# Performance work log

Measured on AMD Instinct MI355X. Metric: run time of the kernel, lower is better.

## Reference

```python
import jax, jax.numpy as jnp
import numpy as np

K = 3          # deform conv kernel size
PAD = 1        # (K-1)//2
DG = 4         # deformable groups
C_IN = 256     # sum(in_channel_list)
C_OUT = 256


def setup_inputs() -> dict:
    key = jax.random.key(0)
    k0, k1, k2, k3, k4, k5 = jax.random.split(key, 6)
    B, H, W = 2, 64, 256
    x0 = jax.random.normal(k0, (B, 64, H, W), dtype=jnp.float32)
    x1 = jax.random.normal(k1, (B, 64, H, W), dtype=jnp.float32)
    x2 = jax.random.normal(k2, (B, 128, H, W), dtype=jnp.float32)
    # conv_offset: 1x1 conv, weight zero-inited in the module; we use small
    # random weights so offsets are spatially varying (nontrivial sampling).
    w_off = jax.random.normal(k3, (DG * K * K * 2, C_IN), dtype=jnp.float32) * 0.01
    b_off = jax.random.normal(k4, (DG * K * K * 2,), dtype=jnp.float32) * 0.5
    # deform conv weight [O, C, K*K] (flat kernel, row-major i*K+j), no bias (mmcv DeformConv)
    w_def = jax.random.normal(k5, (C_OUT, C_IN, K * K), dtype=jnp.float32) / np.sqrt(C_IN * K * K)
    return {"x0": x0, "x1": x1, "x2": x2, "w_off": w_off, "b_off": b_off, "w_def": w_def}


def _deform_gather(xg, py, px):
    # xg: [B, DG, Cg, H, W] grouped input; py/px: [B, DG, K2, H, W] abs sample coords
    B, dg, Cg, H, W = xg.shape
    K2 = py.shape[2]
    y0f = jnp.floor(py)
    x0f = jnp.floor(px)
    wy = py - y0f  # fractional parts
    wx = px - x0f
    y0 = y0f.astype(jnp.int32)
    x0 = x0f.astype(jnp.int32)
    xf = xg.reshape(B, dg, Cg, H * W)

    def corner(yi, xi, w):
        valid = ((yi >= 0) & (yi <= H - 1) & (xi >= 0) & (xi <= W - 1)).astype(xg.dtype)
        idx = jnp.clip(yi, 0, H - 1) * W + jnp.clip(xi, 0, W - 1)   # [B,dg,K2,H,W]
        idxf = idx.reshape(B, dg, 1, K2 * H * W)
        g = jnp.take_along_axis(xf, jnp.broadcast_to(idxf, (B, dg, Cg, K2 * H * W)), axis=-1)
        g = g.reshape(B, dg, Cg, K2, H, W)
        return g * (w * valid)[:, :, None]  # broadcast over Cg

    return (corner(y0, x0, (1.0 - wy) * (1.0 - wx))
            + corner(y0, x0 + 1, (1.0 - wy) * wx)
            + corner(y0 + 1, x0, wy * (1.0 - wx))
            + corner(y0 + 1, x0 + 1, wy * wx))  # [B,dg,Cg,K2,H,W]


def reference(x0, x1, x2, w_off, b_off, w_def):
    x = jnp.concatenate([x0, x1, x2], axis=1)  # [B, C, H, W]
    B, C, H, W = x.shape
    # 1x1 offset conv
    off = jnp.einsum('bchw,oc->bohw', x, w_off) + b_off[None, :, None, None]
    off = off.reshape(B, DG, K * K, 2, H, W)
    dy = off[:, :, :, 0]  # [B,DG,K2,H,W]
    dx = off[:, :, :, 1]
    ky, kx = jnp.meshgrid(jnp.arange(K), jnp.arange(K), indexing='ij')
    ky = ky.reshape(-1).astype(jnp.float32)
    kx = kx.reshape(-1).astype(jnp.float32)
    hh = jnp.arange(H, dtype=jnp.float32)
    ww = jnp.arange(W, dtype=jnp.float32)
    py = hh[None, None, None, :, None] - PAD + ky[None, None, :, None, None] + dy
    px = ww[None, None, None, None, :] - PAD + kx[None, None, :, None, None] + dx
    xg = x.reshape(B, DG, C // DG, H, W)
    samp = _deform_gather(xg, py, px).reshape(B, C, K * K, H, W)
    out = jnp.einsum('bckhw,ock->bohw', samp, w_def)
    return jax.nn.relu(out)
```

## Files before the change

kernel.cpp:

```cpp
#include <hip/hip_runtime.h>


constexpr int H_ = 64, W_ = 256;
constexpr int HWsz = H_ * W_;
constexpr int OC_ = 256;
constexpr int WMAIN_ELEMS = 72 * 16 * 64 * 8;
constexpr int WOFFB_ELEMS = 8 * 5 * 64 * 8;
constexpr size_t XT_ELEMS = (size_t)8 * HWsz * 64;

using f32x4 = __attribute__((ext_vector_type(4))) float;
using s16x8 = __attribute__((ext_vector_type(8))) short;
using u16x8 = __attribute__((ext_vector_type(8))) unsigned short;

__device__ __forceinline__ unsigned short f2bf(float f) {
    unsigned u = __float_as_uint(f);
    return (unsigned short)((u + 0x7fffu + ((u >> 16) & 1u)) >> 16);
}
__device__ __forceinline__ float bf2f(unsigned short u) {
    return __uint_as_float((unsigned)u << 16);
}
__device__ __forceinline__ unsigned cvt_pk_bf16(float lo, float hi) {
    unsigned r;
    asm("v_cvt_pk_bf16_f32 %0, %1, %2" : "=v"(r) : "v"(lo), "v"(hi));
    return r;
}
__device__ __forceinline__ void gload_lds16(const void* g, void* l) {
    __builtin_amdgcn_global_load_lds(
        (const __attribute__((address_space(1))) void*)g,
        (__attribute__((address_space(3))) void*)l, 16, 0, 0);
}


__global__ __launch_bounds__(256) void wprep_kernel(const float* __restrict__ w_def,
                                                    const float* __restrict__ w_off,
                                                    unsigned short* __restrict__ w2) {
    int i = blockIdx.x * 256 + threadIdx.x;
    if (i < WMAIN_ELEMS) {
        int j = i & 7, lane = (i >> 3) & 63, t = (i >> 9) & 15, gkh = i >> 13;
        int half = gkh & 1, gk = gkh >> 1;
        int k = gk % 9, g = gk / 9;
        int oc = t * 16 + (lane & 15);
        int cin = g * 64 + half * 32 + (lane >> 4) * 8 + j;
        w2[i] = f2bf(w_def[(size_t)oc * 2304 + (size_t)cin * 9 + k]);
    } else if (i < WMAIN_ELEMS + WOFFB_ELEMS) {
        int i2 = i - WMAIN_ELEMS;
        int j = i2 & 7, lane = (i2 >> 3) & 63, idx = i2 >> 9;
        int t = idx % 5, c8 = idx / 5;
        int o = t * 16 + (lane & 15);
        int ch = c8 * 32 + (lane >> 4) * 8 + j;
        float v = (o < 72) ? w_off[o * 256 + ch] : 0.f;
        w2[i] = f2bf(v);
    }
}

__global__ __launch_bounds__(256) void xprep_kernel(const float* __restrict__ x0,
                                                    const float* __restrict__ x1,
                                                    const float* __restrict__ x2,
                                                    unsigned short* __restrict__ xt) {
    __shared__ unsigned short tl[256][66];
    const int bg = blockIdx.x >> 6;
    const int y  = blockIdx.x & 63;
    const int b  = bg >> 2, g = bg & 3;
    const int tid = threadIdx.x;
    const float* src = (g == 0) ? x0 + (size_t)b * 64 * HWsz
                     : (g == 1) ? x1 + (size_t)b * 64 * HWsz
                     : x2 + (size_t)b * 128 * HWsz + (size_t)(g - 2) * 64 * HWsz;
    src += y * W_;
    for (int c = 0; c < 64; ++c)
        tl[tid][c] = f2bf(src[(size_t)c * HWsz + tid]);
    __syncthreads();
    unsigned short* dst = xt + ((size_t)bg * HWsz + y * W_) * 64;
    #pragma unroll
    for (int s = 0; s < 8; ++s) {
        int si = s * 256 + tid;
        int px = si >> 3, q = si & 7;
        u16x8 v;
        #pragma unroll
        for (int j = 0; j < 8; ++j) v[j] = tl[px][q * 8 + j];
        *(u16x8*)(dst + (size_t)px * 64 + q * 8) = v;
    }
}


struct GPre {
    float w00, w01, w10, w11;
    u16x8 c00, c01, c10, c11;
};

__global__ __launch_bounds__(512, 4) void deform64_kernel(
    const unsigned short* __restrict__ xt, const float* __restrict__ b_off,
    const unsigned short* __restrict__ w2, float* __restrict__ out)
{
    __shared__ float off_lds[72 * 64];
    __shared__ __align__(16) unsigned short Bbuf[16384];
    __shared__ __align__(16) unsigned short sbuf16[8192];

    const int tid  = threadIdx.x;
    const int lane = tid & 63;
    const int wv   = tid >> 6;
    const int bid  = ((blockIdx.x & 7) << 6) | (blockIdx.x >> 3);
    const int xt4  = bid & 3;
    const int h    = (bid >> 2) & 63;
    const int b    = bid >> 8;
    const int xbase = xt4 * 64;
    const int nh   = wv & 1;
    const int pg   = wv >> 1;
    const int p16  = lane & 15;
    const int cq   = lane >> 4;
    const int bp   = wv * 8 + (lane >> 3);
    const int chg  = lane & 7;
    const int halfw = chg >> 2;
    const int cqw   = chg & 3;
    const int slotw = ((cqw << 4) | (bp & 15)) ^ cqw ^ (halfw << 2);
    const int sbw   = halfw * 2048 + (bp >> 4) * 512 + slotw * 8;
    const int roff0 = pg * 512 + (lane ^ cq) * 8;
    const int roff1 = 2048 + pg * 512 + (lane ^ cq ^ 4) * 8;

    const unsigned short* xtb = xt + (size_t)b * 4 * HWsz * 64;

    if (wv < 4) {
        f32x4 oa[5];
        #pragma unroll
        for (int t = 0; t < 5; ++t) {
            int o = t * 16 + p16;
            float bv = (o < 72) ? b_off[o] : 0.f;
            oa[t][0] = bv; oa[t][1] = bv; oa[t][2] = bv; oa[t][3] = bv;
        }
        const int pixg = h * W_ + xbase + wv * 16;
        #pragma unroll
        for (int c8 = 0; c8 < 8; ++c8) {
            const unsigned short* ap = xtb + (size_t)(c8 >> 1) * HWsz * 64
                                     + (size_t)(pixg + p16) * 64 + (c8 & 1) * 32 + cq * 8;
            s16x8 a = *(const s16x8*)ap;
            const unsigned short* wb = w2 + WMAIN_ELEMS + (size_t)(c8 * 5) * 512;
            #pragma unroll
            for (int t = 0; t < 5; ++t) {
                s16x8 bf = *(const s16x8*)(wb + t * 512 + lane * 8);
                oa[t] = __builtin_amdgcn_mfma_f32_16x16x32_bf16(a, bf, oa[t], 0, 0, 0);
            }
        }
        #pragma unroll
        for (int t = 0; t < 5; ++t) {
            int o = t * 16 + p16;
            if (o < 72) {
                #pragma unroll
                for (int r = 0; r < 4; ++r)
                    off_lds[o * 64 + wv * 16 + cq * 4 + r] = oa[t][r];
            }
        }
    }
    __syncthreads();

    auto stageB = [&](int gk) {
        const char* src = (const char*)w2 + (size_t)gk * 32768 + (size_t)tid * 16;
        char* dst = (char*)&Bbuf[0] + wv * 1024;
        #pragma unroll
        for (int q = 0; q < 4; ++q)
            gload_lds16(src + q * 8192, dst + q * 8192);
    };
    auto gpre = [&](int gk) -> GPre {
        const int k = gk % 9, g = gk / 9;
        const int ky = k / 3, kx = k % 3;
        float dy = off_lds[(2 * gk) * 64 + bp];
        float dx = off_lds[(2 * gk + 1) * 64 + bp];
        float fy = (float)(h - 1 + ky) + dy;
        float fx = (float)(xbase + bp - 1 + kx) + dx;
        float y0f = floorf(fy), x0f = floorf(fx);
        float wy = fy - y0f, wx = fx - x0f;
        int iy0 = (int)y0f, ix0 = (int)x0f;
        int iy1 = iy0 + 1, ix1 = ix0 + 1;
        float vy0 = (iy0 >= 0 && iy0 < H_) ? 1.f : 0.f;
        float vy1 = (iy1 >= 0 && iy1 < H_) ? 1.f : 0.f;
        float vx0 = (ix0 >= 0 && ix0 < W_) ? 1.f : 0.f;
        float vx1 = (ix1 >= 0 && ix1 < W_) ? 1.f : 0.f;
        GPre G;
        G.w00 = (1.f - wy) * (1.f - wx) * vy0 * vx0;
        G.w01 = (1.f - wy) * wx * vy0 * vx1;
        G.w10 = wy * (1.f - wx) * vy1 * vx0;
        G.w11 = wy * wx * vy1 * vx1;
        int cy0 = min(max(iy0, 0), H_ - 1), cy1 = min(max(iy1, 0), H_ - 1);
        int cx0 = min(max(ix0, 0), W_ - 1), cx1 = min(max(ix1, 0), W_ - 1);
        const unsigned short* src = xtb + (size_t)g * HWsz * 64 + chg * 8;
        G.c00 = *(const u16x8*)(src + (cy0 * W_ + cx0) * 64);
        G.c01 = *(const u16x8*)(src + (cy0 * W_ + cx1) * 64);
        G.c10 = *(const u16x8*)(src + (cy1 * W_ + cx0) * 64);
        G.c11 = *(const u16x8*)(src + (cy1 * W_ + cx1) * 64);
        return G;
    };
    auto gpost = [&](const GPre& G, int buf) {
        unsigned d[4];
        #pragma unroll
        for (int q = 0; q < 4; ++q) {
            float v0 = fmaf(G.w00, bf2f(G.c00[2*q]), fmaf(G.w01, bf2f(G.c01[2*q]),
                       fmaf(G.w10, bf2f(G.c10[2*q]), G.w11 * bf2f(G.c11[2*q]))));
            float v1 = fmaf(G.w00, bf2f(G.c00[2*q+1]), fmaf(G.w01, bf2f(G.c01[2*q+1]),
                       fmaf(G.w10, bf2f(G.c10[2*q+1]), G.w11 * bf2f(G.c11[2*q+1]))));
            d[q] = cvt_pk_bf16(v0, v1);
        }
        uint4 v4; v4.x = d[0]; v4.y = d[1]; v4.z = d[2]; v4.w = d[3];
        *(uint4*)&sbuf16[buf * 4096 + sbw] = v4;
    };

    f32x4 acc[8];
    #pragma unroll
    for (int t = 0; t < 8; ++t) { acc[t][0]=0; acc[t][1]=0; acc[t][2]=0; acc[t][3]=0; }

    stageB(0);
    {
        GPre G0 = gpre(0);
        gpost(G0, 0);
    }
    GPre G = gpre(1);

    for (int i = 0; i < 36; ++i) {
        __syncthreads();
        const int cur = i & 1;
        const unsigned short* sb = sbuf16 + cur * 4096;
        {
            s16x8 a = *(const s16x8*)(sb + roff0);
            const unsigned short* bb = Bbuf + nh * 4096 + lane * 8;
            #pragma unroll
            for (int t = 0; t < 8; ++t) {
                s16x8 bf = *(const s16x8*)(bb + t * 512);
                acc[t] = __builtin_amdgcn_mfma_f32_16x16x32_bf16(a, bf, acc[t], 0, 0, 0);
            }
        }
        {
            s16x8 a = *(const s16x8*)(sb + roff1);
            const unsigned short* bb = Bbuf + 8192 + nh * 4096 + lane * 8;
            #pragma unroll
            for (int t = 0; t < 8; ++t) {
                s16x8 bf = *(const s16x8*)(bb + t * 512);
                acc[t] = __builtin_amdgcn_mfma_f32_16x16x32_bf16(a, bf, acc[t], 0, 0, 0);
            }
        }
        if (i < 35) gpost(G, cur ^ 1);
        __syncthreads();
        if (i < 35) stageB(i + 1);
        if (i < 34) G = gpre(i + 2);
    }

    const size_t obase = (size_t)b * OC_ * HWsz + (size_t)h * W_
                       + xbase + pg * 16 + cq * 4;
    #pragma unroll
    for (int t = 0; t < 8; ++t) {
        int oc = nh * 128 + t * 16 + p16;
        float4 r;
        r.x = fmaxf(acc[t][0], 0.f);
        r.y = fmaxf(acc[t][1], 0.f);
        r.z = fmaxf(acc[t][2], 0.f);
        r.w = fmaxf(acc[t][3], 0.f);
        *(float4*)(out + obase + (size_t)oc * HWsz) = r;
    }
}


struct Geom {
    float w00, w01, w10, w11;
    int o00, o01, o10, o11;
    const float* base;
};

__device__ __forceinline__ Geom make_geom(
    int gkh, const float* offp, int h, int wbase, int p, int cq,
    const float* xA, const float* xB, const float* xC)
{
    const int half = gkh & 1, gk = gkh >> 1;
    const int k = gk % 9, g = gk / 9;
    const int ky = k / 3, kx = k % 3;
    float dy = offp[(2 * gk) * 16 + p];
    float dx = offp[(2 * gk + 1) * 16 + p];
    float fy = (float)(h - 1 + ky) + dy;
    float fx = (float)(wbase + p - 1 + kx) + dx;
    float y0f = floorf(fy), x0f = floorf(fx);
    float wy = fy - y0f, wx = fx - x0f;
    int iy0 = (int)y0f, ix0 = (int)x0f;
    int iy1 = iy0 + 1, ix1 = ix0 + 1;
    float vy0 = (iy0 >= 0 && iy0 < H_) ? 1.f : 0.f;
    float vy1 = (iy1 >= 0 && iy1 < H_) ? 1.f : 0.f;
    float vx0 = (ix0 >= 0 && ix0 < W_) ? 1.f : 0.f;
    float vx1 = (ix1 >= 0 && ix1 < W_) ? 1.f : 0.f;
    Geom gm;
    gm.w00 = (1.f - wy) * (1.f - wx) * vy0 * vx0;
    gm.w01 = (1.f - wy) * wx * vy0 * vx1;
    gm.w10 = wy * (1.f - wx) * vy1 * vx0;
    gm.w11 = wy * wx * vy1 * vx1;
    int cy0 = min(max(iy0, 0), H_ - 1), cy1 = min(max(iy1, 0), H_ - 1);
    int cx0 = min(max(ix0, 0), W_ - 1), cx1 = min(max(ix1, 0), W_ - 1);
    int choff = (half * 32 + cq * 8) * HWsz;
    gm.o00 = choff + cy0 * W_ + cx0;
    gm.o01 = choff + cy0 * W_ + cx1;
    gm.o10 = choff + cy1 * W_ + cx0;
    gm.o11 = choff + cy1 * W_ + cx1;
    gm.base = (g == 0) ? xA : (g == 1) ? xB : (g == 2) ? xC : xC + (size_t)64 * HWsz;
    return gm;
}

#define GATHER(J, Cv) do { \
    Cv.x = gm.base[gm.o00 + (J) * HWsz]; \
    Cv.y = gm.base[gm.o01 + (J) * HWsz]; \
    Cv.z = gm.base[gm.o10 + (J) * HWsz]; \
    Cv.w = gm.base[gm.o11 + (J) * HWsz]; \
} while (0)

#define COMB(Cv, IDX) \
    a[IDX] = (short)f2bf(fmaf(w00c, Cv.x, fmaf(w01c, Cv.y, fmaf(w10c, Cv.z, w11c * Cv.w))))

template<bool USE_WS>
__global__ __launch_bounds__(128, 3) void deform_kernel(
    const float* __restrict__ x0, const float* __restrict__ x1,
    const float* __restrict__ x2,
    const float* __restrict__ w_off, const float* __restrict__ b_off,
    const float* __restrict__ w_def, const unsigned short* __restrict__ w2,
    float* __restrict__ out)
{
    __shared__ float off_lds[2][72 * 16];

    const int tid  = threadIdx.x;
    const int lane = tid & 63;
    const int wv   = tid >> 6;
    const int bid  = ((blockIdx.x & 7) << 8) | (blockIdx.x >> 3);
    const int nh   = wv;
    const int ws_  = bid & 15;
    const int h    = (bid >> 4) & 63;
    const int b    = bid >> 10;
    const int p    = lane & 15;
    const int cq   = lane >> 4;
    const int wbase = ws_ * 16;
    const int pix  = h * W_ + wbase;

    const float* xA = x0 + (size_t)b * 64  * HWsz;
    const float* xB = x1 + (size_t)b * 64  * HWsz;
    const float* xC = x2 + (size_t)b * 128 * HWsz;

    f32x4 oa[5];
    #pragma unroll
    for (int t = 0; t < 5; ++t) {
        int o = t * 16 + p;
        float bv = (o < 72) ? b_off[o] : 0.f;
        oa[t][0] = bv; oa[t][1] = bv; oa[t][2] = bv; oa[t][3] = bv;
    }
    #pragma unroll
    for (int c8 = 0; c8 < 8; ++c8) {
        const float* src = (c8 < 2) ? xA + (size_t)c8 * 32 * HWsz
                         : (c8 < 4) ? xB + (size_t)(c8 - 2) * 32 * HWsz
                                    : xC + (size_t)(c8 - 4) * 32 * HWsz;
        s16x8 a;
        #pragma unroll
        for (int j = 0; j < 8; ++j)
            a[j] = (short)f2bf(src[(cq * 8 + j) * HWsz + pix + p]);
        #pragma unroll
        for (int t = 0; t < 5; ++t) {
            int o = t * 16 + p;
            s16x8 bf;
            if (USE_WS) {
                bf = *(const s16x8*)(w2 + WMAIN_ELEMS + (size_t)(c8 * 5 + t) * 512 + lane * 8);
            } else {
                #pragma unroll
                for (int j = 0; j < 8; ++j)
                    bf[j] = (o < 72) ? (short)f2bf(w_off[o * 256 + c8 * 32 + cq * 8 + j])
                                     : (short)0;
            }
            oa[t] = __builtin_amdgcn_mfma_f32_16x16x32_bf16(a, bf, oa[t], 0, 0, 0);
        }
    }
    #pragma unroll
    for (int t = 0; t < 5; ++t) {
        int o = t * 16 + p;
        if (o < 72) {
            #pragma unroll
            for (int r = 0; r < 4; ++r)
                off_lds[wv][o * 16 + cq * 4 + r] = oa[t][r];
        }
    }

    f32x4 acc0={0,0,0,0},acc1={0,0,0,0},acc2={0,0,0,0},acc3={0,0,0,0};
    f32x4 acc4={0,0,0,0},acc5={0,0,0,0},acc6={0,0,0,0},acc7={0,0,0,0};
    const float* offp = &off_lds[wv][0];

    for (int gkh = 0; gkh < 72; ++gkh) {
        Geom gm = make_geom(gkh, offp, h, wbase, p, cq, xA, xB, xC);
        float4 c0, c1, c2, c3, c4, c5, c6, c7;
        GATHER(0, c0); GATHER(1, c1); GATHER(2, c2); GATHER(3, c3);
        GATHER(4, c4); GATHER(5, c5); GATHER(6, c6); GATHER(7, c7);
        float w00c = gm.w00, w01c = gm.w01, w10c = gm.w10, w11c = gm.w11;
        s16x8 a;
        COMB(c0, 0); COMB(c1, 1); COMB(c2, 2); COMB(c3, 3);
        COMB(c4, 4); COMB(c5, 5); COMB(c6, 6); COMB(c7, 7);
        const int half = gkh & 1, gk = gkh >> 1;
        const int k = gk % 9, g = gk / 9;
        const int cbase = g * 64 + half * 32 + cq * 8;
        f32x4* accp[8] = {&acc0,&acc1,&acc2,&acc3,&acc4,&acc5,&acc6,&acc7};
        #pragma unroll
        for (int t = 0; t < 8; ++t) {
            int oc = nh * 128 + t * 16 + p;
            s16x8 bf;
            if (USE_WS) {
                bf = *(const s16x8*)(w2 + gkh * 8192 + nh * 4096 + t * 512 + lane * 8);
            } else {
                #pragma unroll
                for (int j = 0; j < 8; ++j)
                    bf[j] = (short)f2bf(w_def[(size_t)oc * 2304 + (size_t)(cbase + j) * 9 + k]);
            }
            *accp[t] = __builtin_amdgcn_mfma_f32_16x16x32_bf16(a, bf, *accp[t], 0, 0, 0);
        }
    }

    const size_t obase = (size_t)b * OC_ * HWsz + (size_t)h * W_ + wbase + cq * 4;
    f32x4 accs[8] = {acc0, acc1, acc2, acc3, acc4, acc5, acc6, acc7};
    #pragma unroll
    for (int t = 0; t < 8; ++t) {
        int oc = nh * 128 + t * 16 + p;
        float4 r;
        r.x = fmaxf(accs[t][0], 0.f);
        r.y = fmaxf(accs[t][1], 0.f);
        r.z = fmaxf(accs[t][2], 0.f);
        r.w = fmaxf(accs[t][3], 0.f);
        *(float4*)(out + obase + (size_t)oc * HWsz) = r;
    }
}

extern "C" void kernel_launch(void* const* d_in, const int* in_sizes, int n_in,
                              void* d_out, int out_size, void* d_ws, size_t ws_size,
                              hipStream_t stream) {
    const float* x0    = (const float*)d_in[0];
    const float* x1    = (const float*)d_in[1];
    const float* x2    = (const float*)d_in[2];
    const float* w_off = (const float*)d_in[3];
    const float* b_off = (const float*)d_in[4];
    const float* w_def = (const float*)d_in[5];
    float* out = (float*)d_out;

    const size_t w2_bytes   = (size_t)(WMAIN_ELEMS + WOFFB_ELEMS) * 2;
    const size_t full_bytes = (XT_ELEMS + WMAIN_ELEMS + WOFFB_ELEMS) * 2;

    if (ws_size >= full_bytes) {
        unsigned short* xt = (unsigned short*)d_ws;
        unsigned short* w2 = xt + XT_ELEMS;
        hipLaunchKernelGGL(xprep_kernel, dim3(512), dim3(256), 0, stream, x0, x1, x2, xt);
        hipLaunchKernelGGL(wprep_kernel, dim3((WMAIN_ELEMS + WOFFB_ELEMS) / 256), dim3(256),
                           0, stream, w_def, w_off, w2);
        hipLaunchKernelGGL(deform64_kernel, dim3(512), dim3(512), 0, stream,
                           xt, b_off, w2, out);
    } else if (ws_size >= w2_bytes) {
        unsigned short* w2 = (unsigned short*)d_ws;
        hipLaunchKernelGGL(wprep_kernel, dim3((WMAIN_ELEMS + WOFFB_ELEMS) / 256), dim3(256),
                           0, stream, w_def, w_off, w2);
        hipLaunchKernelGGL((deform_kernel<true>), dim3(2048), dim3(128), 0, stream,
                           x0, x1, x2, w_off, b_off, w_def, w2, out);
    } else {
        hipLaunchKernelGGL((deform_kernel<false>), dim3(2048), dim3(128), 0, stream,
                           x0, x1, x2, w_off, b_off, w_def, (const unsigned short*)nullptr, out);
    }
}
```

Before: 91.09 us.

## Precompute packed bilinear geometry in LDS and use packed FP32 FMA for interpolation

```diff
diff --git a/kernel.cpp b/kernel.cpp
--- a/kernel.cpp
+++ b/kernel.cpp
@@ -9,6 +9,7 @@
 constexpr size_t XT_ELEMS = (size_t)8 * HWsz * 64;
 
 using f32x4 = __attribute__((ext_vector_type(4))) float;
+using f32x2 = __attribute__((ext_vector_type(2))) float;
 using s16x8 = __attribute__((ext_vector_type(8))) short;
 using u16x8 = __attribute__((ext_vector_type(8))) unsigned short;
 
@@ -22,6 +23,22 @@
 __device__ __forceinline__ unsigned cvt_pk_bf16(float lo, float hi) {
     unsigned r;
     asm("v_cvt_pk_bf16_f32 %0, %1, %2" : "=v"(r) : "v"(lo), "v"(hi));
+    return r;
+}
+__device__ __forceinline__ f32x2 pk_fma(f32x2 a, f32x2 b, f32x2 c) {
+    f32x2 d;
+    asm("v_pk_fma_f32 %0, %1, %2, %3" : "=v"(d) : "v"(a), "v"(b), "v"(c));
+    return d;
+}
+__device__ __forceinline__ f32x2 pk_mul(f32x2 a, f32x2 b) {
+    f32x2 d;
+    asm("v_pk_mul_f32 %0, %1, %2" : "=v"(d) : "v"(a), "v"(b));
+    return d;
+}
+__device__ __forceinline__ f32x2 unpk_bf(unsigned u) {
+    f32x2 r;
+    r[0] = __uint_as_float(u << 16);
+    r[1] = __uint_as_float(u & 0xffff0000u);
     return r;
 }
 __device__ __forceinline__ void gload_lds16(const void* g, void* l) {
@@ -91,7 +108,7 @@
     const unsigned short* __restrict__ xt, const float* __restrict__ b_off,
     const unsigned short* __restrict__ w2, float* __restrict__ out)
 {
-    __shared__ float off_lds[72 * 64];
+    __shared__ __align__(8) unsigned geomLds[2 * 2304];
     __shared__ __align__(16) unsigned short Bbuf[16384];
     __shared__ __align__(16) unsigned short sbuf16[8192];
 
@@ -118,6 +135,7 @@
 
     const unsigned short* xtb = xt + (size_t)b * 4 * HWsz * 64;
 
+    float* tmpoff = (float*)&Bbuf[0];
     if (wv < 4) {
         f32x4 oa[5];
         #pragma unroll
@@ -145,26 +163,20 @@
             if (o < 72) {
                 #pragma unroll
                 for (int r = 0; r < 4; ++r)
-                    off_lds[o * 64 + wv * 16 + cq * 4 + r] = oa[t][r];
+                    tmpoff[o * 64 + wv * 16 + cq * 4 + r] = oa[t][r];
             }
         }
     }
     __syncthreads();
 
-    auto stageB = [&](int gk) {
-        const char* src = (const char*)w2 + (size_t)gk * 32768 + (size_t)tid * 16;
-        char* dst = (char*)&Bbuf[0] + wv * 1024;
-        #pragma unroll
-        for (int q = 0; q < 4; ++q)
-            gload_lds16(src + q * 8192, dst + q * 8192);
-    };
-    auto gpre = [&](int gk) -> GPre {
-        const int k = gk % 9, g = gk / 9;
+    for (int idx = tid; idx < 36 * 64; idx += 512) {
+        const int gk = idx >> 6, p = idx & 63;
+        const int k = gk % 9;
         const int ky = k / 3, kx = k % 3;
-        float dy = off_lds[(2 * gk) * 64 + bp];
-        float dx = off_lds[(2 * gk + 1) * 64 + bp];
+        float dy = tmpoff[(2 * gk) * 64 + p];
+        float dx = tmpoff[(2 * gk + 1) * 64 + p];
         float fy = (float)(h - 1 + ky) + dy;
-        float fx = (float)(xbase + bp - 1 + kx) + dx;
+        float fx = (float)(xbase + p - 1 + kx) + dx;
         float y0f = floorf(fy), x0f = floorf(fx);
         float wy = fy - y0f, wx = fx - x0f;
         int iy0 = (int)y0f, ix0 = (int)x0f;
@@ -173,31 +185,73 @@
         float vy1 = (iy1 >= 0 && iy1 < H_) ? 1.f : 0.f;
         float vx0 = (ix0 >= 0 && ix0 < W_) ? 1.f : 0.f;
         float vx1 = (ix1 >= 0 && ix1 < W_) ? 1.f : 0.f;
-        GPre G;
-        G.w00 = (1.f - wy) * (1.f - wx) * vy0 * vx0;
-        G.w01 = (1.f - wy) * wx * vy0 * vx1;
-        G.w10 = wy * (1.f - wx) * vy1 * vx0;
-        G.w11 = wy * wx * vy1 * vx1;
+        float w00 = (1.f - wy) * (1.f - wx) * vy0 * vx0;
+        float w01 = (1.f - wy) * wx * vy0 * vx1;
+        float w10 = wy * (1.f - wx) * vy1 * vx0;
+        float w11 = wy * wx * vy1 * vx1;
         int cy0 = min(max(iy0, 0), H_ - 1), cy1 = min(max(iy1, 0), H_ - 1);
         int cx0 = min(max(ix0, 0), W_ - 1), cx1 = min(max(ix1, 0), W_ - 1);
+        unsigned q00 = (unsigned)(w00 * 2047.f + 0.5f);
+        unsigned q01 = (unsigned)(w01 * 2047.f + 0.5f);
+        unsigned q10 = (unsigned)(w10 * 2047.f + 0.5f);
+        unsigned q11 = (unsigned)(w11 * 2047.f + 0.5f);
+        unsigned lo = q00 | (q01 << 11) | ((unsigned)cy0 << 22)
+                    | ((unsigned)(cy1 - cy0) << 28);
+        unsigned hi = q10 | (q11 << 11) | ((unsigned)cx0 << 22)
+                    | ((unsigned)(cx1 - cx0) << 30);
+        geomLds[idx * 2]     = lo;
+        geomLds[idx * 2 + 1] = hi;
+    }
+    __syncthreads();
+
+    auto stageB = [&](int gk) {
+        const char* src = (const char*)w2 + (size_t)gk * 32768 + (size_t)tid * 16;
+        char* dst = (char*)&Bbuf[0] + wv * 1024;
+        #pragma unroll
+        for (int q = 0; q < 4; ++q)
+            gload_lds16(src + q * 8192, dst + q * 8192);
+    };
+    auto gpre = [&](int gk) -> GPre {
+        const int g = gk / 9;
+        const unsigned lo = geomLds[(gk * 64 + bp) * 2];
+        const unsigned hi = geomLds[(gk * 64 + bp) * 2 + 1];
+        GPre G;
+        constexpr float S = 1.f / 2047.f;
+        G.w00 = (float)(lo & 2047u) * S;
+        G.w01 = (float)((lo >> 11) & 2047u) * S;
+        G.w10 = (float)(hi & 2047u) * S;
+        G.w11 = (float)((hi >> 11) & 2047u) * S;
+        const int cy0 = (lo >> 22) & 63;
+        const int cx0 = (hi >> 22) & 255;
+        const int dy1 = ((lo >> 28) & 1) << 14;
+        const int dx1 = ((hi >> 30) & 1) << 6;
+        const int o00 = (cy0 << 14) + (cx0 << 6);
         const unsigned short* src = xtb + (size_t)g * HWsz * 64 + chg * 8;
-        G.c00 = *(const u16x8*)(src + (cy0 * W_ + cx0) * 64);
-        G.c01 = *(const u16x8*)(src + (cy0 * W_ + cx1) * 64);
-        G.c10 = *(const u16x8*)(src + (cy1 * W_ + cx0) * 64);
-        G.c11 = *(const u16x8*)(src + (cy1 * W_ + cx1) * 64);
+        G.c00 = *(const u16x8*)(src + o00);
+        G.c01 = *(const u16x8*)(src + o00 + dx1);
+        G.c10 = *(const u16x8*)(src + o00 + dy1);
+        G.c11 = *(const u16x8*)(src + o00 + dy1 + dx1);
         return G;
     };
     auto gpost = [&](const GPre& G, int buf) {
-        unsigned d[4];
-        #pragma unroll
-        for (int q = 0; q < 4; ++q) {
-            float v0 = fmaf(G.w00, bf2f(G.c00[2*q]), fmaf(G.w01, bf2f(G.c01[2*q]),
-                       fmaf(G.w10, bf2f(G.c10[2*q]), G.w11 * bf2f(G.c11[2*q]))));
-            float v1 = fmaf(G.w00, bf2f(G.c00[2*q+1]), fmaf(G.w01, bf2f(G.c01[2*q+1]),
-                       fmaf(G.w10, bf2f(G.c10[2*q+1]), G.w11 * bf2f(G.c11[2*q+1]))));
-            d[q] = cvt_pk_bf16(v0, v1);
-        }
-        uint4 v4; v4.x = d[0]; v4.y = d[1]; v4.z = d[2]; v4.w = d[3];
+        f32x2 W00 = {G.w00, G.w00}, W01 = {G.w01, G.w01};
+        f32x2 W10 = {G.w10, G.w10}, W11 = {G.w11, G.w11};
+        auto lerp2 = [&](unsigned u00, unsigned u01, unsigned u10, unsigned u11) {
+            f32x2 v = pk_mul(W11, unpk_bf(u11));
+            v = pk_fma(W10, unpk_bf(u10), v);
+            v = pk_fma(W01, unpk_bf(u01), v);
+            v = pk_fma(W00, unpk_bf(u00), v);
+            return cvt_pk_bf16(v[0], v[1]);
+        };
+        const unsigned* q00 = (const unsigned*)&G.c00;
+        const unsigned* q01 = (const unsigned*)&G.c01;
+        const unsigned* q10 = (const unsigned*)&G.c10;
+        const unsigned* q11 = (const unsigned*)&G.c11;
+        uint4 v4;
+        v4.x = lerp2(q00[0], q01[0], q10[0], q11[0]);
+        v4.y = lerp2(q00[1], q01[1], q10[1], q11[1]);
+        v4.z = lerp2(q00[2], q01[2], q10[2], q11[2]);
+        v4.w = lerp2(q00[3], q01[3], q10[3], q11[3]);
         *(uint4*)&sbuf16[buf * 4096 + sbw] = v4;
     };
 
```

New measurement: 132.5 us. +45.5%, slower.
